# Performance work log

Measured on AMD Instinct MI355X. Metric: run time of the kernel, lower is better.

Reference implementation:

```python
import jax, jax.numpy as jnp
import numpy as np

NUM_ITEMS = 50000
IN_FEATS = 64
H_FEATS = 64
NUM_EDGES = 800000


def setup_inputs() -> dict:
    key = jax.random.key(0)
    ks = jax.random.split(key, 12)
    s_in = 1.0 / np.sqrt(IN_FEATS)
    s_h = 1.0 / np.sqrt(H_FEATS)
    return {
        "embed": jax.random.normal(ks[0], (NUM_ITEMS, IN_FEATS), jnp.float32),
        "W1_self": jax.random.normal(ks[1], (IN_FEATS, H_FEATS), jnp.float32) * s_in,
        "W1_neigh": jax.random.normal(ks[2], (IN_FEATS, H_FEATS), jnp.float32) * s_in,
        "b1": jax.random.normal(ks[3], (H_FEATS,), jnp.float32) * s_in,
        "W2_self": jax.random.normal(ks[4], (H_FEATS, H_FEATS), jnp.float32) * s_h,
        "W2_neigh": jax.random.normal(ks[5], (H_FEATS, H_FEATS), jnp.float32) * s_h,
        "b2": jax.random.normal(ks[6], (H_FEATS,), jnp.float32) * s_h,
        "W_fc": jax.random.normal(ks[7], (H_FEATS, IN_FEATS), jnp.float32) * s_h,
        "b_fc": jax.random.normal(ks[8], (IN_FEATS,), jnp.float32) * s_h,
        "item_ids": jnp.arange(NUM_ITEMS, dtype=jnp.int64),
        "src": jax.random.randint(ks[9], (NUM_EDGES,), 0, NUM_ITEMS, jnp.int64),
        "dst": jax.random.randint(ks[10], (NUM_EDGES,), 0, NUM_ITEMS, jnp.int64),
    }


def _sage_mean(h, src, dst, W_self, W_neigh, b, num_nodes):
    # gather src features along edges, mean-reduce into dst nodes
    agg = jax.ops.segment_sum(h[src], dst, num_segments=num_nodes)  # [N, d]
    deg = jax.ops.segment_sum(jnp.ones_like(dst, dtype=h.dtype), dst,
                              num_segments=num_nodes)
    h_neigh = agg / jnp.clip(deg, 1.0, None)[:, None]  # zero for isolated nodes
    return h @ W_self + h_neigh @ W_neigh + b


def reference(embed, W1_self, W1_neigh, b1, W2_self, W2_neigh, b2,
              W_fc, b_fc, item_ids, src, dst):
    n = embed.shape[0]
    x = embed[item_ids]                                   # embedding lookup [N, in]
    h = _sage_mean(x, src, dst, W1_self, W1_neigh, b1, n)  # SAGEConv 1
    h = jax.nn.relu(h)
    h = _sage_mean(h, src, dst, W2_self, W2_neigh, b2, n)  # SAGEConv 2
    return h @ W_fc + b_fc                                 # final linear
```

## Files before the change

kernel.cpp:

```cpp
#include <hip/hip_runtime.h>

#define NN 50000
#define NE 800000
#define F  64
#define SCAN_B 49

typedef float f32x4 __attribute__((ext_vector_type(4)));
typedef float f32x2 __attribute__((ext_vector_type(2)));

__device__ __forceinline__ unsigned bf16rne(float f) {
    unsigned u = __float_as_uint(f);
    return (u + 0x7fffu + ((u >> 16) & 1u)) >> 16;
}
__device__ __forceinline__ float bflo(unsigned p) { return __uint_as_float(p << 16); }
__device__ __forceinline__ float bfhi(unsigned p) { return __uint_as_float(p & 0xffff0000u); }
__device__ __forceinline__ f32x2 up2(unsigned p) {
    f32x2 r;
    r.x = __uint_as_float(p << 16);
    r.y = __uint_as_float(p & 0xffff0000u);
    return r;
}

__device__ __forceinline__ int nswz(int f, int n) { return f * 64 + (n ^ (((f >> 3) & 3) << 3)); }
__device__ __forceinline__ int aswz(int r, int n) { return r * 64 + (n ^ (((r >> 2) & 3) << 3)); }


__launch_bounds__(256)
__global__ void k_count_gather(const int* __restrict__ dst, int* __restrict__ cnt,
                               unsigned short* __restrict__ pos,
                               const float* __restrict__ embed, const int* __restrict__ ids,
                               uint2* __restrict__ xb) {
    int t = blockIdx.x * blockDim.x + threadIdx.x;
    if (t < NE) pos[t] = (unsigned short)atomicAdd(&cnt[dst[t]], 1);
    if (t < NN * 16) {
        int i = t >> 4, c = t & 15;
        float4 v = ((const float4*)embed)[ids[i] * 16 + c];
        uint2 p;
        p.x = bf16rne(v.x) | (bf16rne(v.y) << 16);
        p.y = bf16rne(v.z) | (bf16rne(v.w) << 16);
        xb[t] = p;
    }
}


__launch_bounds__(256)
__global__ void k_scan_a(const int* __restrict__ cnt, int* __restrict__ partials) {
    __shared__ int sc[256];
    int t = threadIdx.x;
    int base = blockIdx.x * 1024 + t * 4;
    int s = 0;
#pragma unroll
    for (int k = 0; k < 4; ++k) {
        int idx = base + k;
        s += (idx < NN) ? cnt[idx] : 0;
    }
    sc[t] = s;
    __syncthreads();
    for (int d = 128; d > 0; d >>= 1) {
        if (t < d) sc[t] += sc[t + d];
        __syncthreads();
    }
    if (t == 0) partials[blockIdx.x] = sc[0];
}

__launch_bounds__(256)
__global__ void k_scan_c2(const int* __restrict__ cnt, const int* __restrict__ partials,
                          int* __restrict__ offs) {
    __shared__ int sboff;
    __shared__ int stotal;
    __shared__ int sc[256];
    int t = threadIdx.x;
    if (t < 64) {
        int v = (t < SCAN_B) ? partials[t] : 0;
        int orig = v;
        for (int d = 1; d < 64; d <<= 1) {
            int u = __shfl_up(v, d);
            if (t >= d) v += u;
        }
        if (t == (int)blockIdx.x) sboff = v - orig;
        if (t == 63) stotal = v;
    }
    int base = blockIdx.x * 1024 + t * 4;
    int v4[4];
#pragma unroll
    for (int k = 0; k < 4; ++k) {
        int idx = base + k;
        v4[k] = (idx < NN) ? cnt[idx] : 0;
    }
    int lsum = v4[0] + v4[1] + v4[2] + v4[3];
    sc[t] = lsum;
    __syncthreads();
    for (int d = 1; d < 256; d <<= 1) {
        int u = (t >= d) ? sc[t - d] : 0;
        __syncthreads();
        sc[t] += u;
        __syncthreads();
    }
    int run = sboff + sc[t] - lsum;
#pragma unroll
    for (int k = 0; k < 4; ++k) {
        int idx = base + k;
        if (idx < NN) { offs[idx] = run; run += v4[k]; }
    }
    if (blockIdx.x == 0 && t == 0) offs[NN] = stotal;
}

__global__ void k_fill(const int* __restrict__ src, const int* __restrict__ dst,
                       const int* __restrict__ offs, const unsigned short* __restrict__ pos,
                       unsigned short* __restrict__ csr) {
    int e = blockIdx.x * blockDim.x + threadIdx.x;
    if (e < NE) csr[offs[dst[e]] + (int)pos[e]] = (unsigned short)src[e];
}


__device__ __forceinline__ void add8(f32x2 s[4], const uint4 v) {
    s[0] += up2(v.x);
    s[1] += up2(v.y);
    s[2] += up2(v.z);
    s[3] += up2(v.w);
}

template <bool LAST>
__launch_bounds__(512)
__global__ void k_fused(const uint4* __restrict__ Ab, const int* __restrict__ offs,
                        const unsigned short* __restrict__ csr,
                        const float* __restrict__ Ws, const float* __restrict__ Wn,
                        const float* __restrict__ b,
                        const float* __restrict__ Wfc, const float* __restrict__ bfc,
                        uint2* __restrict__ outb, float* __restrict__ out) {
    __shared__ alignas(16) float    NsT[F * 64];
    __shared__ alignas(16) unsigned Apk[32 * 64];
    __shared__ alignas(16) unsigned Wpk[F * F];

    const int tid = threadIdx.x;
    const int node0 = blockIdx.x * 64;

    for (int i = tid; i < F * F; i += 512)
        Wpk[i] = bf16rne(Ws[i]) | (bf16rne(Wn[i]) << 16);

    {
        const int n = tid >> 3;
        const int c = tid & 7;
        const int lane = tid & 63;
        const int base = lane & 56;
        const int gnode = node0 + n;
        f32x2 s[4];
        s[0] = 0.f; s[1] = 0.f; s[2] = 0.f; s[3] = 0.f;
        uint4 a = make_uint4(0u, 0u, 0u, 0u);
        float inv = 0.f;
        if (gnode < NN) {
            a = Ab[gnode * 8 + c];
            int beg = offs[gnode], end = offs[gnode + 1];
            int j = beg;
            for (; j + 8 <= end; j += 8) {
                int v = (int)csr[j + c];
                int i0 = __shfl(v, base + 0, 64), i1 = __shfl(v, base + 1, 64);
                int i2 = __shfl(v, base + 2, 64), i3 = __shfl(v, base + 3, 64);
                int i4 = __shfl(v, base + 4, 64), i5 = __shfl(v, base + 5, 64);
                int i6 = __shfl(v, base + 6, 64), i7 = __shfl(v, base + 7, 64);
                uint4 d0 = Ab[i0 * 8 + c], d1 = Ab[i1 * 8 + c];
                uint4 d2 = Ab[i2 * 8 + c], d3 = Ab[i3 * 8 + c];
                uint4 d4 = Ab[i4 * 8 + c], d5 = Ab[i5 * 8 + c];
                uint4 d6 = Ab[i6 * 8 + c], d7 = Ab[i7 * 8 + c];
                add8(s, d0); add8(s, d1); add8(s, d2); add8(s, d3);
                add8(s, d4); add8(s, d5); add8(s, d6); add8(s, d7);
            }
            int rem = end - j;
            if (rem > 0) {
                int v = (int)csr[j + (c < rem ? c : 0)];
                int idx[8];
#pragma unroll
                for (int k = 0; k < 8; ++k) idx[k] = __shfl(v, base + k, 64);
#pragma unroll
                for (int k = 0; k < 8; ++k)
                    if (k < rem) { uint4 d = Ab[idx[k] * 8 + c]; add8(s, d); }
            }
            int deg = end - beg;
            inv = (deg > 0) ? 1.f / (float)deg : 0.f;
        }
        const int f = 8 * c;
        Apk[aswz(4 * c + 0, n)] = a.x;
        Apk[aswz(4 * c + 1, n)] = a.y;
        Apk[aswz(4 * c + 2, n)] = a.z;
        Apk[aswz(4 * c + 3, n)] = a.w;
#pragma unroll
        for (int q = 0; q < 4; ++q) {
            NsT[nswz(f + 2 * q + 0, n)] = s[q].x * inv;
            NsT[nswz(f + 2 * q + 1, n)] = s[q].y * inv;
        }
    }
    __syncthreads();

    const int tx = tid & 15, ty = tid >> 4;
    f32x2 acc[2][2];
    {
        f32x2 b01, b23;
        b01.x = b[4 * tx + 0]; b01.y = b[4 * tx + 1];
        b23.x = b[4 * tx + 2]; b23.y = b[4 * tx + 3];
        acc[0][0] = b01; acc[0][1] = b23;
        acc[1][0] = b01; acc[1][1] = b23;
    }
#pragma unroll 4
    for (int r = 0; r < 32; ++r) {
        const int k0 = 2 * r;
        uint2  ap = *(const uint2*)&Apk[aswz(r, 2 * ty)];
        float2 n0 = *(const float2*)&NsT[nswz(k0, 2 * ty)];
        float2 n1 = *(const float2*)&NsT[nswz(k0 + 1, 2 * ty)];
        uint4  w0 = *(const uint4*)&Wpk[k0 * 64 + 4 * tx];
        uint4  w1 = *(const uint4*)&Wpk[(k0 + 1) * 64 + 4 * tx];
        f32x2 ws0A, ws0B, wn0A, wn0B, ws1A, ws1B, wn1A, wn1B;
        ws0A.x = bflo(w0.x); ws0A.y = bflo(w0.y); ws0B.x = bflo(w0.z); ws0B.y = bflo(w0.w);
        wn0A.x = bfhi(w0.x); wn0A.y = bfhi(w0.y); wn0B.x = bfhi(w0.z); wn0B.y = bfhi(w0.w);
        ws1A.x = bflo(w1.x); ws1A.y = bflo(w1.y); ws1B.x = bflo(w1.z); ws1B.y = bflo(w1.w);
        wn1A.x = bfhi(w1.x); wn1A.y = bfhi(w1.y); wn1B.x = bfhi(w1.z); wn1B.y = bfhi(w1.w);
        const float a00 = bflo(ap.x), a01 = bfhi(ap.x);
        const float a10 = bflo(ap.y), a11 = bfhi(ap.y);
        acc[0][0] += a00 * ws0A + n0.x * wn0A;
        acc[0][1] += a00 * ws0B + n0.x * wn0B;
        acc[1][0] += a10 * ws0A + n0.y * wn0A;
        acc[1][1] += a10 * ws0B + n0.y * wn0B;
        acc[0][0] += a01 * ws1A + n1.x * wn1A;
        acc[0][1] += a01 * ws1B + n1.x * wn1B;
        acc[1][0] += a11 * ws1A + n1.y * wn1A;
        acc[1][1] += a11 * ws1B + n1.y * wn1B;
    }

    if (!LAST) {
#pragma unroll
        for (int i = 0; i < 2; ++i) {
            int node = node0 + 2 * ty + i;
            if (node < NN) {
                float o0 = acc[i][0].x > 0.f ? acc[i][0].x : 0.f;
                float o1 = acc[i][0].y > 0.f ? acc[i][0].y : 0.f;
                float o2 = acc[i][1].x > 0.f ? acc[i][1].x : 0.f;
                float o3 = acc[i][1].y > 0.f ? acc[i][1].y : 0.f;
                uint2 p;
                p.x = bf16rne(o0) | (bf16rne(o1) << 16);
                p.y = bf16rne(o2) | (bf16rne(o3) << 16);
                outb[node * 16 + tx] = p;
            }
        }
    } else {
        __syncthreads();
        float* Wf = (float*)Wpk;
#pragma unroll
        for (int i = 0; i < 2; ++i) {
            NsT[nswz(4 * tx + 0, 2 * ty + i)] = acc[i][0].x;
            NsT[nswz(4 * tx + 1, 2 * ty + i)] = acc[i][0].y;
            NsT[nswz(4 * tx + 2, 2 * ty + i)] = acc[i][1].x;
            NsT[nswz(4 * tx + 3, 2 * ty + i)] = acc[i][1].y;
        }
        for (int i = tid; i < F * F / 4; i += 512)
            ((float4*)Wf)[i] = ((const float4*)Wfc)[i];
        __syncthreads();

        f32x2 acc2[2][2];
        {
            f32x2 b01, b23;
            b01.x = bfc[4 * tx + 0]; b01.y = bfc[4 * tx + 1];
            b23.x = bfc[4 * tx + 2]; b23.y = bfc[4 * tx + 3];
            acc2[0][0] = b01; acc2[0][1] = b23;
            acc2[1][0] = b01; acc2[1][1] = b23;
        }
#pragma unroll 4
        for (int k = 0; k < 64; ++k) {
            float2 a2 = *(const float2*)&NsT[nswz(k, 2 * ty)];
            float4 w4 = *(const float4*)&Wf[k * 64 + 4 * tx];
            f32x2 wA, wB;
            wA.x = w4.x; wA.y = w4.y; wB.x = w4.z; wB.y = w4.w;
            acc2[0][0] += a2.x * wA; acc2[0][1] += a2.x * wB;
            acc2[1][0] += a2.y * wA; acc2[1][1] += a2.y * wB;
        }
#pragma unroll
        for (int i = 0; i < 2; ++i) {
            int node = node0 + 2 * ty + i;
            if (node < NN) {
                f32x4 o;
                o.x = acc2[i][0].x; o.y = acc2[i][0].y;
                o.z = acc2[i][1].x; o.w = acc2[i][1].y;
                __builtin_nontemporal_store(o, (f32x4*)&out[node * 64 + 4 * tx]);
            }
        }
    }
}


extern "C" void kernel_launch(void* const* d_in, const int* in_sizes, int n_in,
                              void* d_out, int out_size, void* d_ws, size_t ws_size,
                              hipStream_t stream) {
    const float* embed = (const float*)d_in[0];
    const float* W1s = (const float*)d_in[1];
    const float* W1n = (const float*)d_in[2];
    const float* b1  = (const float*)d_in[3];
    const float* W2s = (const float*)d_in[4];
    const float* W2n = (const float*)d_in[5];
    const float* b2  = (const float*)d_in[6];
    const float* Wfc = (const float*)d_in[7];
    const float* bfc = (const float*)d_in[8];
    const int* ids = (const int*)d_in[9];
    const int* src = (const int*)d_in[10];
    const int* dst = (const int*)d_in[11];
    float* out = (float*)d_out;

    char* ws = (char*)d_ws;
    size_t off = 0;
    auto alloc = [&](size_t nb) {
        char* p = ws + off;
        off = (off + nb + 255) & ~(size_t)255;
        return p;
    };
    int*   cnt      = (int*)alloc(NN * sizeof(int));
    size_t zero_bytes = off;
    int*   offs     = (int*)alloc((NN + 1) * sizeof(int));
    int*   partials = (int*)alloc(SCAN_B * sizeof(int));
    unsigned short* pos = (unsigned short*)alloc(NE * sizeof(unsigned short));
    unsigned short* csr = (unsigned short*)alloc(NE * sizeof(unsigned short));
    uint2* xb       = (uint2*)alloc((size_t)NN * 16 * sizeof(uint2));
    uint2* h1b      = (uint2*)alloc((size_t)NN * 16 * sizeof(uint2));

    hipMemsetAsync(d_ws, 0, zero_bytes, stream);

    const int TB = 256;
    const int EB = (NE + TB - 1) / TB;
    k_count_gather<<<EB, TB, 0, stream>>>(dst, cnt, pos, embed, ids, xb);
    k_scan_a<<<SCAN_B, 256, 0, stream>>>(cnt, partials);
    k_scan_c2<<<SCAN_B, 256, 0, stream>>>(cnt, partials, offs);
    k_fill<<<EB, TB, 0, stream>>>(src, dst, offs, pos, csr);

    const int NB = (NN + 63) / 64;
    k_fused<false><<<NB, 512, 0, stream>>>((const uint4*)xb, offs, csr,
                                           W1s, W1n, b1, nullptr, nullptr,
                                           h1b, nullptr);
    k_fused<true><<<NB, 512, 0, stream>>>((const uint4*)h1b, offs, csr,
                                          W2s, W2n, b2, Wfc, bfc,
                                          nullptr, out);
}
```

Baseline: 217.1 us.

## Fuse all stages into one cooperative persistent kernel with grid syncs

Replaces the memset plus six kernel launches with a single cooperative kernel that zeroes counts, counts edges, builds CSR, and runs both SAGE layers, separated by grid-wide syncs. The scan is reworked into per-64-node tiles, with each tile recomputing its prefix over all partials. This is meant to remove launch gaps and inter-kernel drain. In exchange the grid is capped at 768 persistent blocks, so tiles loop and grid.sync adds barrier cost. The old multi-kernel path is kept as a fallback.

```diff
diff --git a/kernel.cpp b/kernel.cpp
--- a/kernel.cpp
+++ b/kernel.cpp
@@ -1,8 +1,14 @@
 #include <hip/hip_runtime.h>
+#include <hip/hip_cooperative_groups.h>
+
+namespace cg = cooperative_groups;
 
 #define NN 50000
 #define NE 800000
 #define F  64
+#define NTILE 782
+#define GRID_MAX 768
+#define TPB   512
 #define SCAN_B 49
 
 typedef float f32x4 __attribute__((ext_vector_type(4)));
@@ -24,95 +30,6 @@
 __device__ __forceinline__ int nswz(int f, int n) { return f * 64 + (n ^ (((f >> 3) & 3) << 3)); }
 __device__ __forceinline__ int aswz(int r, int n) { return r * 64 + (n ^ (((r >> 2) & 3) << 3)); }
 
-
-__launch_bounds__(256)
-__global__ void k_count_gather(const int* __restrict__ dst, int* __restrict__ cnt,
-                               unsigned short* __restrict__ pos,
-                               const float* __restrict__ embed, const int* __restrict__ ids,
-                               uint2* __restrict__ xb) {
-    int t = blockIdx.x * blockDim.x + threadIdx.x;
-    if (t < NE) pos[t] = (unsigned short)atomicAdd(&cnt[dst[t]], 1);
-    if (t < NN * 16) {
-        int i = t >> 4, c = t & 15;
-        float4 v = ((const float4*)embed)[ids[i] * 16 + c];
-        uint2 p;
-        p.x = bf16rne(v.x) | (bf16rne(v.y) << 16);
-        p.y = bf16rne(v.z) | (bf16rne(v.w) << 16);
-        xb[t] = p;
-    }
-}
-
-
-__launch_bounds__(256)
-__global__ void k_scan_a(const int* __restrict__ cnt, int* __restrict__ partials) {
-    __shared__ int sc[256];
-    int t = threadIdx.x;
-    int base = blockIdx.x * 1024 + t * 4;
-    int s = 0;
-#pragma unroll
-    for (int k = 0; k < 4; ++k) {
-        int idx = base + k;
-        s += (idx < NN) ? cnt[idx] : 0;
-    }
-    sc[t] = s;
-    __syncthreads();
-    for (int d = 128; d > 0; d >>= 1) {
-        if (t < d) sc[t] += sc[t + d];
-        __syncthreads();
-    }
-    if (t == 0) partials[blockIdx.x] = sc[0];
-}
-
-__launch_bounds__(256)
-__global__ void k_scan_c2(const int* __restrict__ cnt, const int* __restrict__ partials,
-                          int* __restrict__ offs) {
-    __shared__ int sboff;
-    __shared__ int stotal;
-    __shared__ int sc[256];
-    int t = threadIdx.x;
-    if (t < 64) {
-        int v = (t < SCAN_B) ? partials[t] : 0;
-        int orig = v;
-        for (int d = 1; d < 64; d <<= 1) {
-            int u = __shfl_up(v, d);
-            if (t >= d) v += u;
-        }
-        if (t == (int)blockIdx.x) sboff = v - orig;
-        if (t == 63) stotal = v;
-    }
-    int base = blockIdx.x * 1024 + t * 4;
-    int v4[4];
-#pragma unroll
-    for (int k = 0; k < 4; ++k) {
-        int idx = base + k;
-        v4[k] = (idx < NN) ? cnt[idx] : 0;
-    }
-    int lsum = v4[0] + v4[1] + v4[2] + v4[3];
-    sc[t] = lsum;
-    __syncthreads();
-    for (int d = 1; d < 256; d <<= 1) {
-        int u = (t >= d) ? sc[t - d] : 0;
-        __syncthreads();
-        sc[t] += u;
-        __syncthreads();
-    }
-    int run = sboff + sc[t] - lsum;
-#pragma unroll
-    for (int k = 0; k < 4; ++k) {
-        int idx = base + k;
-        if (idx < NN) { offs[idx] = run; run += v4[k]; }
-    }
-    if (blockIdx.x == 0 && t == 0) offs[NN] = stotal;
-}
-
-__global__ void k_fill(const int* __restrict__ src, const int* __restrict__ dst,
-                       const int* __restrict__ offs, const unsigned short* __restrict__ pos,
-                       unsigned short* __restrict__ csr) {
-    int e = blockIdx.x * blockDim.x + threadIdx.x;
-    if (e < NE) csr[offs[dst[e]] + (int)pos[e]] = (unsigned short)src[e];
-}
-
-
 __device__ __forceinline__ void add8(f32x2 s[4], const uint4 v) {
     s[0] += up2(v.x);
     s[1] += up2(v.y);
@@ -121,21 +38,19 @@
 }
 
 template <bool LAST>
-__launch_bounds__(512)
-__global__ void k_fused(const uint4* __restrict__ Ab, const int* __restrict__ offs,
-                        const unsigned short* __restrict__ csr,
-                        const float* __restrict__ Ws, const float* __restrict__ Wn,
-                        const float* __restrict__ b,
-                        const float* __restrict__ Wfc, const float* __restrict__ bfc,
-                        uint2* __restrict__ outb, float* __restrict__ out) {
-    __shared__ alignas(16) float    NsT[F * 64];
-    __shared__ alignas(16) unsigned Apk[32 * 64];
-    __shared__ alignas(16) unsigned Wpk[F * F];
-
+__device__ __forceinline__ void fused_tile(
+    int node0,
+    const uint4* __restrict__ Ab, const int* __restrict__ offs,
+    const unsigned short* __restrict__ csr,
+    const float* __restrict__ Ws, const float* __restrict__ Wn, const float* __restrict__ b,
+    const float* __restrict__ Wfc, const float* __restrict__ bfc,
+    uint2* __restrict__ outb, float* __restrict__ out,
+    float* NsT, unsigned* Apk, unsigned* Wpk)
+{
     const int tid = threadIdx.x;
-    const int node0 = blockIdx.x * 64;
-
-    for (int i = tid; i < F * F; i += 512)
+    __syncthreads();
+
+    for (int i = tid; i < F * F; i += TPB)
         Wpk[i] = bf16rne(Ws[i]) | (bf16rne(Wn[i]) << 16);
 
     {
@@ -250,7 +165,7 @@
             NsT[nswz(4 * tx + 2, 2 * ty + i)] = acc[i][1].x;
             NsT[nswz(4 * tx + 3, 2 * ty + i)] = acc[i][1].y;
         }
-        for (int i = tid; i < F * F / 4; i += 512)
+        for (int i = tid; i < F * F / 4; i += TPB)
             ((float4*)Wf)[i] = ((const float4*)Wfc)[i];
         __syncthreads();
 
@@ -282,6 +197,203 @@
             }
         }
     }
+}
+
+
+__launch_bounds__(TPB)
+__global__ void k_mega(const int* __restrict__ src, const int* __restrict__ dst,
+                       const float* __restrict__ embed, const int* __restrict__ ids,
+                       const float* __restrict__ W1s, const float* __restrict__ W1n,
+                       const float* __restrict__ b1,
+                       const float* __restrict__ W2s, const float* __restrict__ W2n,
+                       const float* __restrict__ b2,
+                       const float* __restrict__ Wfc, const float* __restrict__ bfc,
+                       int* __restrict__ cnt, unsigned short* __restrict__ pos,
+                       int* __restrict__ offs, int* __restrict__ partials,
+                       unsigned short* __restrict__ csr,
+                       uint2* __restrict__ xb, uint2* __restrict__ h1b,
+                       float* __restrict__ out)
+{
+    __shared__ alignas(16) float    NsT[F * 64];
+    __shared__ alignas(16) unsigned Apk[32 * 64];
+    __shared__ alignas(16) unsigned Wpk[F * F];
+
+    cg::grid_group grid = cg::this_grid();
+    const int tid = threadIdx.x;
+    const int gt = blockIdx.x * TPB + tid;
+    const int gstride = gridDim.x * TPB;
+
+    for (int i = gt; i < NN; i += gstride) cnt[i] = 0;
+    grid.sync();
+
+    for (int e = gt; e < NE; e += gstride)
+        pos[e] = (unsigned short)atomicAdd(&cnt[dst[e]], 1);
+    for (int t = gt; t < NN * 16; t += gstride) {
+        int i = t >> 4, c = t & 15;
+        float4 v = ((const float4*)embed)[ids[i] * 16 + c];
+        uint2 p;
+        p.x = bf16rne(v.x) | (bf16rne(v.y) << 16);
+        p.y = bf16rne(v.z) | (bf16rne(v.w) << 16);
+        xb[t] = p;
+    }
+    grid.sync();
+
+    for (int tb = blockIdx.x; tb < NTILE; tb += gridDim.x) {
+        if (tid < 64) {
+            int node = tb * 64 + tid;
+            int v = (node < NN) ? cnt[node] : 0;
+#pragma unroll
+            for (int d = 1; d < 64; d <<= 1) v += __shfl_xor(v, d, 64);
+            if (tid == 0) partials[tb] = v;
+        }
+    }
+    grid.sync();
+
+    for (int tb = blockIdx.x; tb < NTILE; tb += gridDim.x) {
+        if (tid < 64) {
+            int carry = 0, myoff = 0;
+#pragma unroll 1
+            for (int ch = 0; ch < (NTILE + 63) / 64; ++ch) {
+                int idx = ch * 64 + tid;
+                int v = (idx < NTILE) ? partials[idx] : 0;
+                int sc = v;
+#pragma unroll
+                for (int d = 1; d < 64; d <<= 1) {
+                    int u = __shfl_up(sc, d, 64);
+                    if (tid >= d) sc += u;
+                }
+                if (idx == tb) myoff = carry + sc - v;
+                carry += __shfl(sc, 63, 64);
+            }
+            int boff = __shfl(myoff, tb & 63, 64);
+            int node = tb * 64 + tid;
+            int v = (node < NN) ? cnt[node] : 0;
+            int sc = v;
+#pragma unroll
+            for (int d = 1; d < 64; d <<= 1) {
+                int u = __shfl_up(sc, d, 64);
+                if (tid >= d) sc += u;
+            }
+            if (node < NN) offs[node] = boff + sc - v;
+            if (tb == 0 && tid == 0) offs[NN] = carry;
+        }
+    }
+    grid.sync();
+
+    for (int e = gt; e < NE; e += gstride)
+        csr[offs[dst[e]] + (int)pos[e]] = (unsigned short)src[e];
+    grid.sync();
+
+    for (int tb = blockIdx.x; tb < NTILE; tb += gridDim.x)
+        fused_tile<false>(tb * 64, (const uint4*)xb, offs, csr, W1s, W1n, b1,
+                          nullptr, nullptr, h1b, nullptr, NsT, Apk, Wpk);
+    grid.sync();
+
+    for (int tb = blockIdx.x; tb < NTILE; tb += gridDim.x)
+        fused_tile<true>(tb * 64, (const uint4*)h1b, offs, csr, W2s, W2n, b2,
+                         Wfc, bfc, nullptr, out, NsT, Apk, Wpk);
+}
+
+
+__launch_bounds__(256)
+__global__ void k_count_gather(const int* __restrict__ dst, int* __restrict__ cnt,
+                               unsigned short* __restrict__ pos,
+                               const float* __restrict__ embed, const int* __restrict__ ids,
+                               uint2* __restrict__ xb) {
+    int t = blockIdx.x * blockDim.x + threadIdx.x;
+    if (t < NE) pos[t] = (unsigned short)atomicAdd(&cnt[dst[t]], 1);
+    if (t < NN * 16) {
+        int i = t >> 4, c = t & 15;
+        float4 v = ((const float4*)embed)[ids[i] * 16 + c];
+        uint2 p;
+        p.x = bf16rne(v.x) | (bf16rne(v.y) << 16);
+        p.y = bf16rne(v.z) | (bf16rne(v.w) << 16);
+        xb[t] = p;
+    }
+}
+
+__launch_bounds__(256)
+__global__ void k_scan_a(const int* __restrict__ cnt, int* __restrict__ partials) {
+    __shared__ int sc[256];
+    int t = threadIdx.x;
+    int base = blockIdx.x * 1024 + t * 4;
+    int s = 0;
+#pragma unroll
+    for (int k = 0; k < 4; ++k) {
+        int idx = base + k;
+        s += (idx < NN) ? cnt[idx] : 0;
+    }
+    sc[t] = s;
+    __syncthreads();
+    for (int d = 128; d > 0; d >>= 1) {
+        if (t < d) sc[t] += sc[t + d];
+        __syncthreads();
+    }
+    if (t == 0) partials[blockIdx.x] = sc[0];
+}
+
+__launch_bounds__(256)
+__global__ void k_scan_c2(const int* __restrict__ cnt, const int* __restrict__ partials,
+                          int* __restrict__ offs) {
+    __shared__ int sboff;
+    __shared__ int stotal;
+    __shared__ int sc[256];
+    int t = threadIdx.x;
+    if (t < 64) {
+        int v = (t < SCAN_B) ? partials[t] : 0;
+        int orig = v;
+        for (int d = 1; d < 64; d <<= 1) {
+            int u = __shfl_up(v, d);
+            if (t >= d) v += u;
+        }
+        if (t == (int)blockIdx.x) sboff = v - orig;
+        if (t == 63) stotal = v;
+    }
+    int base = blockIdx.x * 1024 + t * 4;
+    int v4[4];
+#pragma unroll
+    for (int k = 0; k < 4; ++k) {
+        int idx = base + k;
+        v4[k] = (idx < NN) ? cnt[idx] : 0;
+    }
+    int lsum = v4[0] + v4[1] + v4[2] + v4[3];
+    sc[t] = lsum;
+    __syncthreads();
+    for (int d = 1; d < 256; d <<= 1) {
+        int u = (t >= d) ? sc[t - d] : 0;
+        __syncthreads();
+        sc[t] += u;
+        __syncthreads();
+    }
+    int run = sboff + sc[t] - lsum;
+#pragma unroll
+    for (int k = 0; k < 4; ++k) {
+        int idx = base + k;
+        if (idx < NN) { offs[idx] = run; run += v4[k]; }
+    }
+    if (blockIdx.x == 0 && t == 0) offs[NN] = stotal;
+}
+
+__global__ void k_fill(const int* __restrict__ src, const int* __restrict__ dst,
+                       const int* __restrict__ offs, const unsigned short* __restrict__ pos,
+                       unsigned short* __restrict__ csr) {
+    int e = blockIdx.x * blockDim.x + threadIdx.x;
+    if (e < NE) csr[offs[dst[e]] + (int)pos[e]] = (unsigned short)src[e];
+}
+
+template <bool LAST>
+__launch_bounds__(TPB)
+__global__ void k_fused(const uint4* __restrict__ Ab, const int* __restrict__ offs,
+                        const unsigned short* __restrict__ csr,
+                        const float* __restrict__ Ws, const float* __restrict__ Wn,
+                        const float* __restrict__ b,
+                        const float* __restrict__ Wfc, const float* __restrict__ bfc,
+                        uint2* __restrict__ outb, float* __restrict__ out) {
+    __shared__ alignas(16) float    NsT[F * 64];
+    __shared__ alignas(16) unsigned Apk[32 * 64];
+    __shared__ alignas(16) unsigned Wpk[F * F];
+    fused_tile<LAST>(blockIdx.x * 64, Ab, offs, csr, Ws, Wn, b, Wfc, bfc,
+                     outb, out, NsT, Apk, Wpk);
 }
 
 
@@ -312,26 +424,52 @@
     int*   cnt      = (int*)alloc(NN * sizeof(int));
     size_t zero_bytes = off;
     int*   offs     = (int*)alloc((NN + 1) * sizeof(int));
-    int*   partials = (int*)alloc(SCAN_B * sizeof(int));
+    int*   partials = (int*)alloc(NTILE * sizeof(int));
     unsigned short* pos = (unsigned short*)alloc(NE * sizeof(unsigned short));
     unsigned short* csr = (unsigned short*)alloc(NE * sizeof(unsigned short));
     uint2* xb       = (uint2*)alloc((size_t)NN * 16 * sizeof(uint2));
     uint2* h1b      = (uint2*)alloc((size_t)NN * 16 * sizeof(uint2));
 
-    hipMemsetAsync(d_ws, 0, zero_bytes, stream);
-
+    static int  s_bpc = -2;
+    static bool s_coop_ok = true;
+
+    if (s_bpc == -2) {
+        int nb = 0;
+        hipError_t e = hipOccupancyMaxActiveBlocksPerMultiprocessor(
+            &nb, (const void*)k_mega, TPB, 0);
+        s_bpc = (e == hipSuccess) ? nb : 0;
+        if (s_bpc <= 0) s_coop_ok = false;
+    }
+
+    if (s_coop_ok) {
+        int grid = s_bpc * 256;
+        if (grid > GRID_MAX) grid = GRID_MAX;
+        void* args[] = {
+            (void*)&src, (void*)&dst, (void*)&embed, (void*)&ids,
+            (void*)&W1s, (void*)&W1n, (void*)&b1,
+            (void*)&W2s, (void*)&W2n, (void*)&b2,
+            (void*)&Wfc, (void*)&bfc,
+            (void*)&cnt, (void*)&pos, (void*)&offs, (void*)&partials, (void*)&csr,
+            (void*)&xb, (void*)&h1b, (void*)&out
+        };
+        hipError_t e = hipLaunchCooperativeKernel((const void*)k_mega, dim3(grid),
+                                                  dim3(TPB), args, 0, stream);
+        if (e == hipSuccess) return;
+        s_coop_ok = false;
+    }
+
+    hipMemsetAsync(cnt, 0, zero_bytes, stream);
     const int TB = 256;
     const int EB = (NE + TB - 1) / TB;
     k_count_gather<<<EB, TB, 0, stream>>>(dst, cnt, pos, embed, ids, xb);
     k_scan_a<<<SCAN_B, 256, 0, stream>>>(cnt, partials);
     k_scan_c2<<<SCAN_B, 256, 0, stream>>>(cnt, partials, offs);
     k_fill<<<EB, TB, 0, stream>>>(src, dst, offs, pos, csr);
-
-    const int NB = (NN + 63) / 64;
-    k_fused<false><<<NB, 512, 0, stream>>>((const uint4*)xb, offs, csr,
+    const int NB = NTILE;
+    k_fused<false><<<NB, TPB, 0, stream>>>((const uint4*)xb, offs, csr,
                                            W1s, W1n, b1, nullptr, nullptr,
                                            h1b, nullptr);
-    k_fused<true><<<NB, 512, 0, stream>>>((const uint4*)h1b, offs, csr,
+    k_fused<true><<<NB, TPB, 0, stream>>>((const uint4*)h1b, offs, csr,
                                           W2s, W2n, b2, Wfc, bfc,
                                           nullptr, out);
 }
```

After: 463.6 us. +113.5%, slower.
